# Kernel optimization log

Hardware: AMD Instinct MI355X
Metric: run time of the kernel (lower is better)

Reference implementation:

```python
import jax, jax.numpy as jnp
import numpy as np

H = 16          # heads_num
D = 1024        # model_dim
HD = D // H     # per-head dim
NEG = -1e9


def setup_inputs() -> dict:
    key = jax.random.key(0)
    ks = jax.random.split(key, 12)
    B, S = 4, 1024
    inp = {
        "q": jax.random.normal(ks[0], (B, S, D), jnp.float32),
        "k": jax.random.normal(ks[1], (B, S, D), jnp.float32),
        "v": jax.random.normal(ks[2], (B, S, D), jnp.float32),
        "mask": jnp.ones((B, 1, S), jnp.int32),
    }
    s = 1.0 / np.sqrt(D)
    inp["Wq"] = jax.random.normal(ks[3], (D, D), jnp.float32) * s
    inp["bq"] = jnp.zeros((D,), jnp.float32)
    inp["Wk"] = jax.random.normal(ks[4], (D, D), jnp.float32) * s
    inp["bk"] = jnp.zeros((D,), jnp.float32)
    inp["Wv"] = jax.random.normal(ks[5], (D, D), jnp.float32) * s
    inp["bv"] = jnp.zeros((D,), jnp.float32)
    inp["Wo"] = jax.random.normal(ks[6], (D, D), jnp.float32) * s
    inp["bo"] = jnp.zeros((D,), jnp.float32)
    return inp


def _split_heads(x, B):
    # [B, S, D] -> [B, H, S, HD]
    return x.reshape(B, -1, H, HD).transpose(0, 2, 1, 3)


def reference(q, k, v, mask, Wq, bq, Wk, bk, Wv, bv, Wo, bo):
    B = q.shape[0]
    qh = _split_heads(q @ Wq.T + bq, B)  # [B,H,Sq,HD]
    kh = _split_heads(k @ Wk.T + bk, B)  # [B,H,Sk,HD]
    vh = _split_heads(v @ Wv.T + bv, B)  # [B,H,Sk,HD]
    scores = jnp.einsum("bhqd,bhkd->bhqk", qh, kh) / np.sqrt(HD)
    # mask [B,1,Sk] -> unsqueeze head dim -> [B,1,1,Sk], broadcast over q and heads
    scores = jnp.where(mask[:, None] == 0, NEG, scores)
    attn = jax.nn.softmax(scores, axis=-1)  # dropout in eval mode = identity
    ctx = jnp.einsum("bhqk,bhkd->bhqd", attn, vh)
    out = ctx.transpose(0, 2, 1, 3).reshape(B, -1, D)
    return out @ Wo.T + bo
```

## Files before the change

kernel.cpp:

```cpp
#include <hip/hip_runtime.h>
#include <hip/hip_bf16.h>
#include <math.h>

typedef __bf16 bf16;
typedef __bf16 bf16x8 __attribute__((ext_vector_type(8)));
typedef __bf16 bf16x2 __attribute__((ext_vector_type(2)));
typedef float f32x4 __attribute__((ext_vector_type(4)));
typedef float f32x16 __attribute__((ext_vector_type(16)));

#define D_MODEL 1024
#define SEQ 1024
#define BATCH 4
#define NHEAD 16
#define MTOT (BATCH*SEQ)

#define QSCALE 0.18033688011112042f
#define MASKNEG -1e9f
#define EXP2(x) __builtin_amdgcn_exp2f(x)

__global__ void cast_all(const float* __restrict__ s0, const float* __restrict__ s1,
                         const float* __restrict__ s2, const float* __restrict__ s3,
                         const float* __restrict__ s4, const float* __restrict__ s5,
                         const float* __restrict__ s6,
                         bf16* d0, bf16* d1, bf16* d2, bf16* d3, bf16* d4, bf16* d5, bf16* d6) {
    int z = blockIdx.y;
    const float* s; bf16* d; int n;
    switch (z) {
        case 0: s = s0; d = d0; n = MTOT * D_MODEL; break;
        case 1: s = s1; d = d1; n = MTOT * D_MODEL; break;
        case 2: s = s2; d = d2; n = MTOT * D_MODEL; break;
        case 3: s = s3; d = d3; n = D_MODEL * D_MODEL; break;
        case 4: s = s4; d = d4; n = D_MODEL * D_MODEL; break;
        case 5: s = s5; d = d5; n = D_MODEL * D_MODEL; break;
        default: s = s6; d = d6; n = D_MODEL * D_MODEL; break;
    }
    int idx = (blockIdx.x * blockDim.x + threadIdx.x) * 8;
    int stride = gridDim.x * blockDim.x * 8;
    for (int i = idx; i < n; i += stride) {
        const float4* p = (const float4*)(s + i);
        float4 a = p[0], b = p[1];
        bf16x8 o;
        o[0] = (bf16)a.x; o[1] = (bf16)a.y; o[2] = (bf16)a.z; o[3] = (bf16)a.w;
        o[4] = (bf16)b.x; o[5] = (bf16)b.y; o[6] = (bf16)b.z; o[7] = (bf16)b.w;
        *(bf16x8*)(d + i) = o;
    }
}

template<typename OT, int MODE>
__global__ __launch_bounds__(256, 3)
void gemm_bt(const bf16* __restrict__ A0, const bf16* __restrict__ A1, const bf16* __restrict__ A2,
             const bf16* __restrict__ W0, const bf16* __restrict__ W1, const bf16* __restrict__ W2,
             const float* __restrict__ bias0, const float* __restrict__ bias1, const float* __restrict__ bias2,
             OT* __restrict__ O0, OT* __restrict__ O1, OT* __restrict__ O2) {
    constexpr int BK = 32;
    constexpr int K = D_MODEL;
    constexpr int NT = K / BK;
    __shared__ alignas(16) bf16 As[2][128 * BK];
    __shared__ alignas(16) bf16 Bs[2][128 * BK];

    int z = (MODE == 0) ? blockIdx.z : 0;
    const bf16* A = (z == 0) ? A0 : (z == 1) ? A1 : A2;
    const bf16* W = (z == 0) ? W0 : (z == 1) ? W1 : W2;
    const float* bias = (z == 0) ? bias0 : (z == 1) ? bias1 : bias2;
    OT* Out = (z == 0) ? O0 : (z == 1) ? O1 : O2;

    int tid = threadIdx.x;
    int lane = tid & 63, w = tid >> 6;
    int l15 = lane & 15, l4 = lane >> 4;
    int m0 = blockIdx.x * 128;
    int n0 = blockIdx.y * 128;
    int wm = w >> 1, wn = w & 1;

    f32x4 acc[4][4] = {};

    int srow = lane >> 2;
    int scol = (lane & 3) * 8;

    auto stage = [&](int buf, int kt) {
#pragma unroll
        for (int i = 0; i < 2; ++i) {
            int seg = w * 2 + i;
            int row = seg * 16 + srow;
            const bf16* srcA = A + (size_t)(m0 + row) * K + kt * BK + scol;
            const bf16* srcB = W + (size_t)(n0 + row) * K + kt * BK + scol;
            __builtin_amdgcn_global_load_lds(
                (const __attribute__((address_space(1))) void*)srcA,
                (__attribute__((address_space(3))) void*)(&As[buf][seg * 512]), 16, 0, 0);
            __builtin_amdgcn_global_load_lds(
                (const __attribute__((address_space(1))) void*)srcB,
                (__attribute__((address_space(3))) void*)(&Bs[buf][seg * 512]), 16, 0, 0);
        }
    };

    stage(0, 0);
    __syncthreads();

    for (int kt = 0; kt < NT; ++kt) {
        int cur = kt & 1;
        if (kt + 1 < NT) stage(cur ^ 1, kt + 1);

        const bf16* pa = &As[cur][(wm * 64 + l15) * BK + l4 * 8];
        const bf16* pb = &Bs[cur][(wn * 64 + l15) * BK + l4 * 8];
        bf16x8 af[4], bv[4];
#pragma unroll
        for (int m = 0; m < 4; ++m) af[m] = *(const bf16x8*)(pa + m * 16 * BK);
#pragma unroll
        for (int n = 0; n < 4; ++n) bv[n] = *(const bf16x8*)(pb + n * 16 * BK);
#pragma unroll
        for (int m = 0; m < 4; ++m)
#pragma unroll
            for (int n = 0; n < 4; ++n)
                acc[m][n] = __builtin_amdgcn_mfma_f32_16x16x32_bf16(af[m], bv[n], acc[m][n], 0, 0, 0);

        __syncthreads();
    }

    float bload[4];
#pragma unroll
    for (int n = 0; n < 4; ++n) bload[n] = bias[n0 + wn * 64 + n * 16 + l15];

    if (MODE == 0 && z == 2) {
#pragma unroll
        for (int m = 0; m < 4; ++m) {
            int row = m0 + wm * 64 + m * 16 + l4 * 4;
#pragma unroll
            for (int n = 0; n < 4; ++n) {
                int col = n0 + wn * 64 + n * 16 + l15;
                float bl = bload[n];
#pragma unroll
                for (int r = 0; r < 4; ++r) {
                    float vv = acc[m][n][r] + bl;
                    int rr = row + r;
                    int bb = rr >> 10, s = rr & 1023;
                    Out[((size_t)(bb * 1024 + col)) * 1024 + s] = (OT)vv;
                }
            }
        }
    } else {
        const float sc = (MODE == 0 && z == 0) ? QSCALE : 1.0f;
#pragma unroll
        for (int m = 0; m < 4; ++m) {
            int row = m0 + wm * 64 + m * 16 + l4 * 4;
#pragma unroll
            for (int n = 0; n < 4; ++n) {
                int col = n0 + wn * 64 + n * 16 + l15;
                float bl = bload[n];
#pragma unroll
                for (int r = 0; r < 4; ++r) {
                    float vv = (acc[m][n][r] + bl) * sc;
                    Out[(size_t)(row + r) * D_MODEL + col] = (OT)vv;
                }
            }
        }
    }
}

__device__ __forceinline__ unsigned pkbf(float lo, float hi2) {
    bf16x2 t; t[0] = (bf16)lo; t[1] = (bf16)hi2;
    return __builtin_bit_cast(unsigned, t);
}

__global__ __launch_bounds__(512, 4)
void attn_fwd(const bf16* __restrict__ Qp, const bf16* __restrict__ Kp,
              const bf16* __restrict__ VT, const int* __restrict__ maskp,
              bf16* __restrict__ ctx) {
    __shared__ alignas(16) unsigned char smem[69760];
    bf16* Kbuf = (bf16*)smem;
    bf16* Vbuf = (bf16*)(smem + 32768);
    float* madd2 = (float*)(smem + 65536);
    int* tflag = (int*)(smem + 69632);

    int tid = threadIdx.x;
    int lane = tid & 63, w = tid >> 6;
    int l31 = lane & 31, hi = lane >> 5;
    int hh = w >> 2, wl = w & 3;

    int fid = blockIdx.x;
    int xcd = fid & 7, idx = fid >> 3;
    int by = xcd * 8 + (idx >> 3);
    int bx = idx & 7;
    int b = by >> 4, h = by & 15;
    int q0 = bx * 128;

    {
        madd2[tid] = maskp[b * SEQ + tid] ? 0.f : MASKNEG;
        madd2[512 + tid] = maskp[b * SEQ + 512 + tid] ? 0.f : MASKNEG;
#pragma unroll
        for (int i = 0; i < 2; ++i) {
            int t = w * 2 + i;
            unsigned long long bl = __ballot(maskp[b * SEQ + t * 64 + lane] != 0);
            if (lane == 0) tflag[t] = (bl == ~0ull);
        }
    }

    bf16x8 qf[4];
    {
        const bf16* qb = Qp + ((size_t)(b * SEQ + q0 + wl * 32 + l31)) * D_MODEL + h * 64 + hi * 8;
#pragma unroll
        for (int ks = 0; ks < 4; ++ks) qf[ks] = *(const bf16x8*)(qb + ks * 16);
    }

    f32x16 oacc0 = {}, oacc1 = {};
    float lsum = 0.f;

    auto stage = [&](int buf, int t) {
        int kv0 = (hh * 8 + t) * 64;
        bf16* Kd = Kbuf + (size_t)(buf * 2 + hh) * 4096;
        bf16* Vd = Vbuf + (size_t)(buf * 2 + hh) * 4096;
#pragma unroll
        for (int i = 0; i < 2; ++i) {
            int seg = wl * 2 + i;
            int row = seg * 8 + (lane >> 3);
            int cs = ((lane & 7) ^ (row & 7)) * 8;
            const bf16* srcK = Kp + ((size_t)(b * SEQ + kv0 + row)) * D_MODEL + h * 64 + cs;
            __builtin_amdgcn_global_load_lds(
                (const __attribute__((address_space(1))) void*)srcK,
                (__attribute__((address_space(3))) void*)(Kd + seg * 512), 16, 0, 0);
            const bf16* srcV = VT + ((size_t)(b * 1024 + h * 64 + row)) * SEQ + kv0 + cs;
            __builtin_amdgcn_global_load_lds(
                (const __attribute__((address_space(1))) void*)srcV,
                (__attribute__((address_space(3))) void*)(Vd + seg * 512), 16, 0, 0);
        }
    };

    auto half_p = [&](f32x16& p, const float* mbh, int flag, const bf16* Vl, int ksb) -> float {
        float a0 = 0.f, a1 = 0.f, a2 = 0.f, a3 = 0.f;
        if (flag) {
#pragma unroll
            for (int g = 0; g < 4; ++g) {
                float s0 = 0.f;
#pragma unroll
                for (int c = 0; c < 4; ++c) {
                    int r = g * 4 + c;
                    float e = EXP2(p[r]);
                    p[r] = e; s0 += e;
                }
                if (g == 0) a0 = s0; else if (g == 1) a1 = s0;
                else if (g == 2) a2 = s0; else a3 = s0;
            }
        } else {
#pragma unroll
            for (int g = 0; g < 4; ++g) {
                f32x4 mk = *(const f32x4*)(mbh + g * 8 + hi * 4);
                float s0 = 0.f;
#pragma unroll
                for (int c = 0; c < 4; ++c) {
                    int r = g * 4 + c;
                    float e = EXP2(p[r] + mk[c]);
                    p[r] = e; s0 += e;
                }
                if (g == 0) a0 = s0; else if (g == 1) a1 = s0;
                else if (g == 2) a2 = s0; else a3 = s0;
            }
        }
        union FragU { bf16x8 v; unsigned u[4]; };
        FragU A0, A1;
#define PKSW(PV, RA, RB, DST)  { \
            unsigned a_ = pkbf(PV[RA], PV[(RA) + 1]); \
            unsigned b_ = pkbf(PV[RB], PV[(RB) + 1]); \
            auto rr_ = __builtin_amdgcn_permlane32_swap(a_, b_, false, false); \
            DST.u[((RA) & 3) >> 1] = rr_[0]; DST.u[(((RA) & 3) >> 1) + 2] = rr_[1]; }
        PKSW(p, 0, 4,  A0);
        PKSW(p, 2, 6,  A0);
        PKSW(p, 8, 12, A1);
        PKSW(p, 10, 14, A1);
#undef PKSW
        __builtin_amdgcn_s_setprio(1);
#pragma unroll
        for (int i = 0; i < 2; ++i) {
            int ks = ksb + i;
            bf16x8 pav = i ? A1.v : A0.v;
            int sl = ((2 * ks + hi) ^ (l31 & 7)) * 8;
            bf16x8 v0 = *(const bf16x8*)(&Vl[l31 * 64 + sl]);
            bf16x8 v1 = *(const bf16x8*)(&Vl[(32 + l31) * 64 + sl]);
            oacc0 = __builtin_amdgcn_mfma_f32_32x32x16_bf16(pav, v0, oacc0, 0, 0, 0);
            oacc1 = __builtin_amdgcn_mfma_f32_32x32x16_bf16(pav, v1, oacc1, 0, 0, 0);
        }
        __builtin_amdgcn_s_setprio(0);
        return (a0 + a1) + (a2 + a3);
    };

    stage(0, 0);
    __syncthreads();

    for (int t = 0; t < 8; ++t) {
        int cur = t & 1;
        if (t + 1 < 8) stage(cur ^ 1, t + 1);
        int kt = hh * 8 + t;
        const bf16* Kl = Kbuf + (size_t)(cur * 2 + hh) * 4096;
        const bf16* Vl = Vbuf + (size_t)(cur * 2 + hh) * 4096;
        const float* mb = &madd2[kt * 64];
        int flag = tflag[kt];

        float ts;
        {
            f32x16 p = {};
            __builtin_amdgcn_s_setprio(1);
#pragma unroll
            for (int ks = 0; ks < 4; ++ks) {
                int sl = ((2 * ks + hi) ^ (l31 & 7)) * 8;
                bf16x8 k0 = *(const bf16x8*)(&Kl[l31 * 64 + sl]);
                p = __builtin_amdgcn_mfma_f32_32x32x16_bf16(k0, qf[ks], p, 0, 0, 0);
            }
            __builtin_amdgcn_s_setprio(0);
            ts = half_p(p, mb, flag, Vl, 0);
        }
        {
            f32x16 p = {};
            __builtin_amdgcn_s_setprio(1);
#pragma unroll
            for (int ks = 0; ks < 4; ++ks) {
                int sl = ((2 * ks + hi) ^ (l31 & 7)) * 8;
                bf16x8 k1 = *(const bf16x8*)(&Kl[(32 + l31) * 64 + sl]);
                p = __builtin_amdgcn_mfma_f32_32x32x16_bf16(k1, qf[ks], p, 0, 0, 0);
            }
            __builtin_amdgcn_s_setprio(0);
            ts += half_p(p, mb + 32, flag, Vl, 2);
        }
        ts += __shfl_xor(ts, 32);
        lsum += ts;

        __syncthreads();
    }

    float* Omrg = (float*)smem;
    float* Lmrg = (float*)(smem + 32768);
    if (hh == 1) {
#pragma unroll
        for (int g = 0; g < 4; ++g) {
#pragma unroll
            for (int c = 0; c < 4; ++c) {
                int r = g * 4 + c;
                int q = c + g * 8 + hi * 4;
                Omrg[wl * 2048 + q * 64 + l31]      = oacc0[r];
                Omrg[wl * 2048 + q * 64 + 32 + l31] = oacc1[r];
            }
        }
        if (hi == 0) Lmrg[wl * 32 + l31] = lsum;
    }
    __syncthreads();
    if (hh == 0) {
        float ltot = lsum + Lmrg[wl * 32 + l31];
#pragma unroll
        for (int g = 0; g < 4; ++g) {
#pragma unroll
            for (int c = 0; c < 4; ++c) {
                int r = g * 4 + c;
                int q = c + g * 8 + hi * 4;
                float o0 = oacc0[r] + Omrg[wl * 2048 + q * 64 + l31];
                float o1 = oacc1[r] + Omrg[wl * 2048 + q * 64 + 32 + l31];
                float sden = __shfl(ltot, q);
                float inv = 1.0f / sden;
                int qg = q0 + wl * 32 + q;
                size_t base = ((size_t)(b * SEQ + qg)) * D_MODEL + h * 64;
                ctx[base + l31]      = (bf16)(o0 * inv);
                ctx[base + 32 + l31] = (bf16)(o1 * inv);
            }
        }
    }
}

extern "C" void kernel_launch(void* const* d_in, const int* in_sizes, int n_in,
                              void* d_out, int out_size, void* d_ws, size_t ws_size,
                              hipStream_t stream) {
    const float* q  = (const float*)d_in[0];
    const float* k  = (const float*)d_in[1];
    const float* v  = (const float*)d_in[2];
    const int* mask = (const int*)d_in[3];
    const float* Wq = (const float*)d_in[4];
    const float* bq = (const float*)d_in[5];
    const float* Wk = (const float*)d_in[6];
    const float* bk = (const float*)d_in[7];
    const float* Wv = (const float*)d_in[8];
    const float* bv = (const float*)d_in[9];
    const float* Wo = (const float*)d_in[10];
    const float* bo = (const float*)d_in[11];
    float* out = (float*)d_out;

    char* ws = (char*)d_ws;
    size_t szQKV = (size_t)MTOT * D_MODEL * sizeof(bf16);
    size_t szW = (size_t)D_MODEL * D_MODEL * sizeof(bf16);
    bf16* qb  = (bf16*)ws; ws += szQKV;
    bf16* kb  = (bf16*)ws; ws += szQKV;
    bf16* vb  = (bf16*)ws; ws += szQKV;
    bf16* Wqb = (bf16*)ws; ws += szW;
    bf16* Wkb = (bf16*)ws; ws += szW;
    bf16* Wvb = (bf16*)ws; ws += szW;
    bf16* Wob = (bf16*)ws; ws += szW;
    bf16* Qp  = (bf16*)ws; ws += szQKV;
    bf16* Kp  = (bf16*)ws; ws += szQKV;
    bf16* VT  = (bf16*)ws; ws += szQKV;
    bf16* ctx = (bf16*)ws; ws += szQKV;

    dim3 gc(512, 7, 1);
    cast_all<<<gc, 256, 0, stream>>>(q, k, v, Wq, Wk, Wv, Wo,
                                     qb, kb, vb, Wqb, Wkb, Wvb, Wob);

    dim3 g1(MTOT / 128, D_MODEL / 128, 3);
    gemm_bt<bf16, 0><<<g1, 256, 0, stream>>>(qb, kb, vb, Wqb, Wkb, Wvb,
                                             bq, bk, bv, Qp, Kp, VT);

    attn_fwd<<<dim3(512), 512, 0, stream>>>(Qp, Kp, VT, mask, ctx);

    dim3 g3(MTOT / 128, D_MODEL / 128, 1);
    gemm_bt<float, 1><<<g3, 256, 0, stream>>>(ctx, ctx, ctx, Wob, Wob, Wob,
                                              bo, bo, bo, out, out, out);
}
```

Baseline: 103.5 us.

## Fuse fp32-to-bf16 activation cast into QKV projection GEMM loads

The separate pass that cast the q/k/v activations to bf16 is removed. The QKV GEMM now streams fp32 activations straight into LDS with an XOR-swizzled layout and converts them to bf16 while building the MFMA fragments. This drops a full read-write round trip of three 16 MB activation tensors plus their bf16 staging buffers, and the cast kernel now only converts the weights. In exchange the QKV GEMM moves twice as many A bytes per tile, uses double the A LDS footprint, and does the conversion in its inner loop, so it may become more memory- or LDS-bound.

Measured after the change: 108.6 us. +5.0%, slower.

```diff
diff --git a/kernel.cpp b/kernel.cpp
--- a/kernel.cpp
+++ b/kernel.cpp
@@ -18,22 +18,18 @@
 #define MASKNEG -1e9f
 #define EXP2(x) __builtin_amdgcn_exp2f(x)
 
-__global__ void cast_all(const float* __restrict__ s0, const float* __restrict__ s1,
-                         const float* __restrict__ s2, const float* __restrict__ s3,
-                         const float* __restrict__ s4, const float* __restrict__ s5,
-                         const float* __restrict__ s6,
-                         bf16* d0, bf16* d1, bf16* d2, bf16* d3, bf16* d4, bf16* d5, bf16* d6) {
+__global__ void cast_w(const float* __restrict__ s0, const float* __restrict__ s1,
+                       const float* __restrict__ s2, const float* __restrict__ s3,
+                       bf16* d0, bf16* d1, bf16* d2, bf16* d3) {
     int z = blockIdx.y;
-    const float* s; bf16* d; int n;
+    const float* s; bf16* d;
     switch (z) {
-        case 0: s = s0; d = d0; n = MTOT * D_MODEL; break;
-        case 1: s = s1; d = d1; n = MTOT * D_MODEL; break;
-        case 2: s = s2; d = d2; n = MTOT * D_MODEL; break;
-        case 3: s = s3; d = d3; n = D_MODEL * D_MODEL; break;
-        case 4: s = s4; d = d4; n = D_MODEL * D_MODEL; break;
-        case 5: s = s5; d = d5; n = D_MODEL * D_MODEL; break;
-        default: s = s6; d = d6; n = D_MODEL * D_MODEL; break;
-    }
+        case 0: s = s0; d = d0; break;
+        case 1: s = s1; d = d1; break;
+        case 2: s = s2; d = d2; break;
+        default: s = s3; d = d3; break;
+    }
+    const int n = D_MODEL * D_MODEL;
     int idx = (blockIdx.x * blockDim.x + threadIdx.x) * 8;
     int stride = gridDim.x * blockDim.x * 8;
     for (int i = idx; i < n; i += stride) {
@@ -46,23 +42,22 @@
     }
 }
 
-template<typename OT, int MODE>
 __global__ __launch_bounds__(256, 3)
-void gemm_bt(const bf16* __restrict__ A0, const bf16* __restrict__ A1, const bf16* __restrict__ A2,
-             const bf16* __restrict__ W0, const bf16* __restrict__ W1, const bf16* __restrict__ W2,
-             const float* __restrict__ bias0, const float* __restrict__ bias1, const float* __restrict__ bias2,
-             OT* __restrict__ O0, OT* __restrict__ O1, OT* __restrict__ O2) {
+void gemm_qkv(const float* __restrict__ A0, const float* __restrict__ A1, const float* __restrict__ A2,
+              const bf16* __restrict__ W0, const bf16* __restrict__ W1, const bf16* __restrict__ W2,
+              const float* __restrict__ bias0, const float* __restrict__ bias1, const float* __restrict__ bias2,
+              bf16* __restrict__ O0, bf16* __restrict__ O1, bf16* __restrict__ O2) {
     constexpr int BK = 32;
     constexpr int K = D_MODEL;
     constexpr int NT = K / BK;
-    __shared__ alignas(16) bf16 As[2][128 * BK];
-    __shared__ alignas(16) bf16 Bs[2][128 * BK];
-
-    int z = (MODE == 0) ? blockIdx.z : 0;
-    const bf16* A = (z == 0) ? A0 : (z == 1) ? A1 : A2;
+    __shared__ alignas(16) float Asf[2][128 * BK];
+    __shared__ alignas(16) bf16  Bs[2][128 * BK];
+
+    int z = blockIdx.z;
+    const float* A = (z == 0) ? A0 : (z == 1) ? A1 : A2;
     const bf16* W = (z == 0) ? W0 : (z == 1) ? W1 : W2;
     const float* bias = (z == 0) ? bias0 : (z == 1) ? bias1 : bias2;
-    OT* Out = (z == 0) ? O0 : (z == 1) ? O1 : O2;
+    bf16* Out = (z == 0) ? O0 : (z == 1) ? O1 : O2;
 
     int tid = threadIdx.x;
     int lane = tid & 63, w = tid >> 6;
@@ -73,6 +68,122 @@
 
     f32x4 acc[4][4] = {};
 
+    int bsrow = lane >> 2;
+    int bscol = (lane & 3) * 8;
+    int arow8 = lane >> 3;
+    int acs = ((lane & 7) ^ (lane >> 3)) * 4;
+
+    auto stage = [&](int buf, int kt) {
+#pragma unroll
+        for (int i = 0; i < 4; ++i) {
+            int seg = w * 4 + i;
+            int row = seg * 8 + arow8;
+            const float* srcA = A + (size_t)(m0 + row) * K + kt * BK + acs;
+            __builtin_amdgcn_global_load_lds(
+                (const __attribute__((address_space(1))) void*)srcA,
+                (__attribute__((address_space(3))) void*)(&Asf[buf][seg * 256]), 16, 0, 0);
+        }
+#pragma unroll
+        for (int i = 0; i < 2; ++i) {
+            int seg = w * 2 + i;
+            int row = seg * 16 + bsrow;
+            const bf16* srcB = W + (size_t)(n0 + row) * K + kt * BK + bscol;
+            __builtin_amdgcn_global_load_lds(
+                (const __attribute__((address_space(1))) void*)srcB,
+                (__attribute__((address_space(3))) void*)(&Bs[buf][seg * 512]), 16, 0, 0);
+        }
+    };
+
+    stage(0, 0);
+    __syncthreads();
+
+    for (int kt = 0; kt < NT; ++kt) {
+        int cur = kt & 1;
+        if (kt + 1 < NT) stage(cur ^ 1, kt + 1);
+
+        bf16x8 af[4];
+#pragma unroll
+        for (int m = 0; m < 4; ++m) {
+            int r = wm * 64 + m * 16 + l15;
+            int p0 = (2 * l4) ^ (r & 7);
+            int p1 = (2 * l4 + 1) ^ (r & 7);
+            f32x4 a0 = *(const f32x4*)(&Asf[cur][r * BK + p0 * 4]);
+            f32x4 a1 = *(const f32x4*)(&Asf[cur][r * BK + p1 * 4]);
+            bf16x8 o;
+            o[0] = (bf16)a0[0]; o[1] = (bf16)a0[1]; o[2] = (bf16)a0[2]; o[3] = (bf16)a0[3];
+            o[4] = (bf16)a1[0]; o[5] = (bf16)a1[1]; o[6] = (bf16)a1[2]; o[7] = (bf16)a1[3];
+            af[m] = o;
+        }
+        const bf16* pb = &Bs[cur][(wn * 64 + l15) * BK + l4 * 8];
+        bf16x8 bv[4];
+#pragma unroll
+        for (int n = 0; n < 4; ++n) bv[n] = *(const bf16x8*)(pb + n * 16 * BK);
+#pragma unroll
+        for (int m = 0; m < 4; ++m)
+#pragma unroll
+            for (int n = 0; n < 4; ++n)
+                acc[m][n] = __builtin_amdgcn_mfma_f32_16x16x32_bf16(af[m], bv[n], acc[m][n], 0, 0, 0);
+
+        __syncthreads();
+    }
+
+    float bload[4];
+#pragma unroll
+    for (int n = 0; n < 4; ++n) bload[n] = bias[n0 + wn * 64 + n * 16 + l15];
+
+    if (z == 2) {
+#pragma unroll
+        for (int m = 0; m < 4; ++m) {
+            int row = m0 + wm * 64 + m * 16 + l4 * 4;
+#pragma unroll
+            for (int n = 0; n < 4; ++n) {
+                int col = n0 + wn * 64 + n * 16 + l15;
+                float bl = bload[n];
+#pragma unroll
+                for (int r = 0; r < 4; ++r) {
+                    float vv = acc[m][n][r] + bl;
+                    int rr = row + r;
+                    int bb = rr >> 10, s = rr & 1023;
+                    Out[((size_t)(bb * 1024 + col)) * 1024 + s] = (bf16)vv;
+                }
+            }
+        }
+    } else {
+        const float sc = (z == 0) ? QSCALE : 1.0f;
+#pragma unroll
+        for (int m = 0; m < 4; ++m) {
+            int row = m0 + wm * 64 + m * 16 + l4 * 4;
+#pragma unroll
+            for (int n = 0; n < 4; ++n) {
+                int col = n0 + wn * 64 + n * 16 + l15;
+                float bl = bload[n];
+#pragma unroll
+                for (int r = 0; r < 4; ++r) {
+                    float vv = (acc[m][n][r] + bl) * sc;
+                    Out[(size_t)(row + r) * D_MODEL + col] = (bf16)vv;
+                }
+            }
+        }
+    }
+}
+
+__global__ __launch_bounds__(256, 3)
+void gemm_out(const bf16* __restrict__ A, const bf16* __restrict__ W,
+              const float* __restrict__ bias, float* __restrict__ Out) {
+    constexpr int BK = 32;
+    constexpr int K = D_MODEL;
+    constexpr int NT = K / BK;
+    __shared__ alignas(16) bf16 As[2][128 * BK];
+    __shared__ alignas(16) bf16 Bs[2][128 * BK];
+
+    int tid = threadIdx.x;
+    int lane = tid & 63, w = tid >> 6;
+    int l15 = lane & 15, l4 = lane >> 4;
+    int m0 = blockIdx.x * 128;
+    int n0 = blockIdx.y * 128;
+    int wm = w >> 1, wn = w & 1;
+
+    f32x4 acc[4][4] = {};
     int srow = lane >> 2;
     int scol = (lane & 3) * 8;
 
@@ -118,39 +229,16 @@
     float bload[4];
 #pragma unroll
     for (int n = 0; n < 4; ++n) bload[n] = bias[n0 + wn * 64 + n * 16 + l15];
-
-    if (MODE == 0 && z == 2) {
-#pragma unroll
-        for (int m = 0; m < 4; ++m) {
-            int row = m0 + wm * 64 + m * 16 + l4 * 4;
-#pragma unroll
-            for (int n = 0; n < 4; ++n) {
-                int col = n0 + wn * 64 + n * 16 + l15;
-                float bl = bload[n];
-#pragma unroll
-                for (int r = 0; r < 4; ++r) {
-                    float vv = acc[m][n][r] + bl;
-                    int rr = row + r;
-                    int bb = rr >> 10, s = rr & 1023;
-                    Out[((size_t)(bb * 1024 + col)) * 1024 + s] = (OT)vv;
-                }
-            }
-        }
-    } else {
-        const float sc = (MODE == 0 && z == 0) ? QSCALE : 1.0f;
-#pragma unroll
-        for (int m = 0; m < 4; ++m) {
-            int row = m0 + wm * 64 + m * 16 + l4 * 4;
-#pragma unroll
-            for (int n = 0; n < 4; ++n) {
-                int col = n0 + wn * 64 + n * 16 + l15;
-                float bl = bload[n];
-#pragma unroll
-                for (int r = 0; r < 4; ++r) {
-                    float vv = (acc[m][n][r] + bl) * sc;
-                    Out[(size_t)(row + r) * D_MODEL + col] = (OT)vv;
-                }
-            }
+#pragma unroll
+    for (int m = 0; m < 4; ++m) {
+        int row = m0 + wm * 64 + m * 16 + l4 * 4;
+#pragma unroll
+        for (int n = 0; n < 4; ++n) {
+            int col = n0 + wn * 64 + n * 16 + l15;
+            float bl = bload[n];
+#pragma unroll
+            for (int r = 0; r < 4; ++r)
+                Out[(size_t)(row + r) * D_MODEL + col] = acc[m][n][r] + bl;
         }
     }
 }
@@ -380,9 +468,6 @@
     char* ws = (char*)d_ws;
     size_t szQKV = (size_t)MTOT * D_MODEL * sizeof(bf16);
     size_t szW = (size_t)D_MODEL * D_MODEL * sizeof(bf16);
-    bf16* qb  = (bf16*)ws; ws += szQKV;
-    bf16* kb  = (bf16*)ws; ws += szQKV;
-    bf16* vb  = (bf16*)ws; ws += szQKV;
     bf16* Wqb = (bf16*)ws; ws += szW;
     bf16* Wkb = (bf16*)ws; ws += szW;
     bf16* Wvb = (bf16*)ws; ws += szW;
@@ -392,17 +477,15 @@
     bf16* VT  = (bf16*)ws; ws += szQKV;
     bf16* ctx = (bf16*)ws; ws += szQKV;
 
-    dim3 gc(512, 7, 1);
-    cast_all<<<gc, 256, 0, stream>>>(q, k, v, Wq, Wk, Wv, Wo,
-                                     qb, kb, vb, Wqb, Wkb, Wvb, Wob);
+    dim3 gc(256, 4, 1);
+    cast_w<<<gc, 256, 0, stream>>>(Wq, Wk, Wv, Wo, Wqb, Wkb, Wvb, Wob);
 
     dim3 g1(MTOT / 128, D_MODEL / 128, 3);
-    gemm_bt<bf16, 0><<<g1, 256, 0, stream>>>(qb, kb, vb, Wqb, Wkb, Wvb,
-                                             bq, bk, bv, Qp, Kp, VT);
+    gemm_qkv<<<g1, 256, 0, stream>>>(q, k, v, Wqb, Wkb, Wvb,
+                                     bq, bk, bv, Qp, Kp, VT);
 
     attn_fwd<<<dim3(512), 512, 0, stream>>>(Qp, Kp, VT, mask, ctx);
 
     dim3 g3(MTOT / 128, D_MODEL / 128, 1);
-    gemm_bt<float, 1><<<g3, 256, 0, stream>>>(ctx, ctx, ctx, Wob, Wob, Wob,
-                                              bo, bo, bo, out, out, out);
-}
+    gemm_out<<<g3, 256, 0, stream>>>(ctx, Wob, bo, out);
+}
```

## Load GEMM operands directly from global into registers, dropping LDS staging

Applied to the files above, without the earlier changes.

Removes the LDS double buffer and the per-iteration barriers from the projection GEMM. Each wave now loads its A and W fragments straight from global memory into registers, with two register sets ping-ponged across k-steps, and raises wave priority around the MFMA block. Launch bounds drop to 2 blocks per CU so the extra registers fit. Loads shared between waves are no longer reused through LDS, which doubles global/L2 traffic and uses uncoalesced 16-byte row-strided accesses.

Result: slower. 165.8 us (+60.2%).

```diff
diff --git a/kernel.cpp b/kernel.cpp
--- a/kernel.cpp
+++ b/kernel.cpp
@@ -47,16 +47,13 @@
 }
 
 template<typename OT, int MODE>
-__global__ __launch_bounds__(256, 3)
+__global__ __launch_bounds__(256, 2)
 void gemm_bt(const bf16* __restrict__ A0, const bf16* __restrict__ A1, const bf16* __restrict__ A2,
              const bf16* __restrict__ W0, const bf16* __restrict__ W1, const bf16* __restrict__ W2,
              const float* __restrict__ bias0, const float* __restrict__ bias1, const float* __restrict__ bias2,
              OT* __restrict__ O0, OT* __restrict__ O1, OT* __restrict__ O2) {
-    constexpr int BK = 32;
     constexpr int K = D_MODEL;
-    constexpr int NT = K / BK;
-    __shared__ alignas(16) bf16 As[2][128 * BK];
-    __shared__ alignas(16) bf16 Bs[2][128 * BK];
+    constexpr int NT = K / 32;
 
     int z = (MODE == 0) ? blockIdx.z : 0;
     const bf16* A = (z == 0) ? A0 : (z == 1) ? A1 : A2;
@@ -71,48 +68,37 @@
     int n0 = blockIdx.y * 128;
     int wm = w >> 1, wn = w & 1;
 
+    const bf16* Ab = A + (size_t)(m0 + wm * 64 + l15) * K + l4 * 8;
+    const bf16* Bb = W + (size_t)(n0 + wn * 64 + l15) * K + l4 * 8;
+
     f32x4 acc[4][4] = {};
-
-    int srow = lane >> 2;
-    int scol = (lane & 3) * 8;
-
-    auto stage = [&](int buf, int kt) {
-#pragma unroll
-        for (int i = 0; i < 2; ++i) {
-            int seg = w * 2 + i;
-            int row = seg * 16 + srow;
-            const bf16* srcA = A + (size_t)(m0 + row) * K + kt * BK + scol;
-            const bf16* srcB = W + (size_t)(n0 + row) * K + kt * BK + scol;
-            __builtin_amdgcn_global_load_lds(
-                (const __attribute__((address_space(1))) void*)srcA,
-                (__attribute__((address_space(3))) void*)(&As[buf][seg * 512]), 16, 0, 0);
-            __builtin_amdgcn_global_load_lds(
-                (const __attribute__((address_space(1))) void*)srcB,
-                (__attribute__((address_space(3))) void*)(&Bs[buf][seg * 512]), 16, 0, 0);
-        }
+    bf16x8 a0[4], b0[4], a1[4], b1[4];
+
+    auto load = [&](bf16x8* av, bf16x8* bv, int kt) {
+#pragma unroll
+        for (int m = 0; m < 4; ++m)
+            av[m] = *(const bf16x8*)(Ab + (size_t)m * 16 * K + kt * 32);
+#pragma unroll
+        for (int n = 0; n < 4; ++n)
+            bv[n] = *(const bf16x8*)(Bb + (size_t)n * 16 * K + kt * 32);
     };
-
-    stage(0, 0);
-    __syncthreads();
-
-    for (int kt = 0; kt < NT; ++kt) {
-        int cur = kt & 1;
-        if (kt + 1 < NT) stage(cur ^ 1, kt + 1);
-
-        const bf16* pa = &As[cur][(wm * 64 + l15) * BK + l4 * 8];
-        const bf16* pb = &Bs[cur][(wn * 64 + l15) * BK + l4 * 8];
-        bf16x8 af[4], bv[4];
-#pragma unroll
-        for (int m = 0; m < 4; ++m) af[m] = *(const bf16x8*)(pa + m * 16 * BK);
-#pragma unroll
-        for (int n = 0; n < 4; ++n) bv[n] = *(const bf16x8*)(pb + n * 16 * BK);
+    auto compute = [&](const bf16x8* av, const bf16x8* bv) {
+        __builtin_amdgcn_s_setprio(1);
 #pragma unroll
         for (int m = 0; m < 4; ++m)
 #pragma unroll
             for (int n = 0; n < 4; ++n)
-                acc[m][n] = __builtin_amdgcn_mfma_f32_16x16x32_bf16(af[m], bv[n], acc[m][n], 0, 0, 0);
-
-        __syncthreads();
+                acc[m][n] = __builtin_amdgcn_mfma_f32_16x16x32_bf16(av[m], bv[n], acc[m][n], 0, 0, 0);
+        __builtin_amdgcn_s_setprio(0);
+    };
+
+    load(a0, b0, 0);
+#pragma unroll 1
+    for (int kt2 = 0; kt2 < NT / 2; ++kt2) {
+        load(a1, b1, 2 * kt2 + 1);
+        compute(a0, b0);
+        if (kt2 + 1 < NT / 2) load(a0, b0, 2 * kt2 + 2);
+        compute(a1, b1);
     }
 
     float bload[4];
```

## Add 256x256 8-wave QKV GEMM with quadrant-interleaved LDS pipelining

Applied to the files above, without the earlier changes.

Replaces the fused QKV projection GEMM with a new kernel using 256x256 tiles, 512 threads, BK=64, XOR-swizzled LDS, and a hand-scheduled pipeline. The pipeline interleaves half-tile global-to-LDS loads with MFMA quadrants, using explicit vmcnt/lgkmcnt waits and setprio. The aim is more data reuse per tile and better overlap of memory with matrix math. In exchange, the grid gets smaller (192 blocks) and register pressure rises, and the hand-tuned wait counts are fragile. The output GEMM is split into its own simpler kernel.

New measurement: 106.2 us. 2.6% more time.

```diff
diff --git a/kernel.cpp b/kernel.cpp
--- a/kernel.cpp
+++ b/kernel.cpp
@@ -17,6 +17,10 @@
 #define QSCALE 0.18033688011112042f
 #define MASKNEG -1e9f
 #define EXP2(x) __builtin_amdgcn_exp2f(x)
+
+#define GLL(SRC, DST) __builtin_amdgcn_global_load_lds( \
+    (const __attribute__((address_space(1))) void*)(SRC), \
+    (__attribute__((address_space(3))) void*)(DST), 16, 0, 0)
 
 __global__ void cast_all(const float* __restrict__ s0, const float* __restrict__ s1,
                          const float* __restrict__ s2, const float* __restrict__ s3,
@@ -46,23 +50,183 @@
     }
 }
 
-template<typename OT, int MODE>
+#define VMBAR  do { asm volatile("s_waitcnt vmcnt(6)" ::: "memory"); \
+                    __builtin_amdgcn_s_barrier(); \
+                    __builtin_amdgcn_sched_barrier(0); } while (0)
+#define LGKM0  do { asm volatile("s_waitcnt lgkmcnt(0)" ::: "memory"); \
+                    __builtin_amdgcn_sched_barrier(0); } while (0)
+
+__global__ __launch_bounds__(512, 2)
+void gemm_qkv8(const bf16* __restrict__ A0p, const bf16* __restrict__ A1p, const bf16* __restrict__ A2p,
+               const bf16* __restrict__ W0, const bf16* __restrict__ W1, const bf16* __restrict__ W2,
+               const float* __restrict__ bias0, const float* __restrict__ bias1, const float* __restrict__ bias2,
+               bf16* __restrict__ O0, bf16* __restrict__ O1, bf16* __restrict__ O2) {
+    constexpr int K = D_MODEL;
+    __shared__ bf16 Al[2][2][8192];
+    __shared__ bf16 Bl[2][2][8192];
+
+    int z = blockIdx.z;
+    const bf16* A = (z == 0) ? A0p : (z == 1) ? A1p : A2p;
+    const bf16* W = (z == 0) ? W0 : (z == 1) ? W1 : W2;
+    const float* bias = (z == 0) ? bias0 : (z == 1) ? bias1 : bias2;
+    bf16* Out = (z == 0) ? O0 : (z == 1) ? O1 : O2;
+
+    int tid = threadIdx.x;
+    int l = tid & 63, w = tid >> 6;
+    int l15 = l & 15, l4 = l >> 4;
+    int wm = w >> 2, wn = w & 3;
+    int m0 = blockIdx.x * 256;
+    int n0 = blockIdx.y * 256;
+
+    f32x4 acc[8][4] = {};
+
+    int srf = l >> 3;
+    int scc = (l & 7) ^ (srf & 7);
+
+    auto stageA = [&](int buf, int H, int kt) {
+#pragma unroll
+        for (int j = 0; j < 2; ++j) {
+            int r = (w * 2 + j) * 8 + srf;
+            const bf16* src = A + (size_t)(m0 + H * 128 + r) * K + kt * 64 + scc * 8;
+            GLL(src, &Al[buf][H][(w * 2 + j) * 512]);
+        }
+    };
+    auto stageB = [&](int buf, int H, int kt) {
+#pragma unroll
+        for (int j = 0; j < 2; ++j) {
+            int r = (w * 2 + j) * 8 + srf;
+            const bf16* src = W + (size_t)(n0 + H * 128 + r) * K + kt * 64 + scc * 8;
+            GLL(src, &Bl[buf][H][(w * 2 + j) * 512]);
+        }
+    };
+
+    bf16x8 a[4][2], bf0[2][2], bf1[2][2];
+
+    auto loadA = [&](int buf, int H) {
+#pragma unroll
+        for (int j2 = 0; j2 < 4; ++j2) {
+            int rh = (2 * j2 + wm) * 16 + l15;
+#pragma unroll
+            for (int ks = 0; ks < 2; ++ks) {
+                int cp = (ks * 4 + l4) ^ (l15 & 7);
+                a[j2][ks] = *(const bf16x8*)&Al[buf][H][rh * 64 + cp * 8];
+            }
+        }
+    };
+    auto loadB = [&](bf16x8 bdst[2][2], int buf, int H) {
+#pragma unroll
+        for (int n2 = 0; n2 < 2; ++n2) {
+            int rh = (4 * n2 + wn) * 16 + l15;
+#pragma unroll
+            for (int ks = 0; ks < 2; ++ks) {
+                int cp = (ks * 4 + l4) ^ (l15 & 7);
+                bdst[n2][ks] = *(const bf16x8*)&Bl[buf][H][rh * 64 + cp * 8];
+            }
+        }
+    };
+
+#define MMAQ(M, N, BSET) do { \
+        __builtin_amdgcn_s_setprio(1); \
+        _Pragma("unroll") \
+        for (int j2 = 0; j2 < 4; ++j2) \
+        _Pragma("unroll") \
+        for (int n2 = 0; n2 < 2; ++n2) \
+        _Pragma("unroll") \
+        for (int ks = 0; ks < 2; ++ks) \
+            acc[(M)*4 + j2][(N)*2 + n2] = __builtin_amdgcn_mfma_f32_16x16x32_bf16( \
+                a[j2][ks], BSET[n2][ks], acc[(M)*4 + j2][(N)*2 + n2], 0, 0, 0); \
+        __builtin_amdgcn_s_setprio(0); \
+    } while (0)
+
+    stageA(0, 0, 0); stageB(0, 0, 0);
+    stageA(0, 1, 0); stageB(0, 1, 0);
+    stageA(1, 0, 1); stageB(1, 0, 1);
+
+#pragma unroll 1
+    for (int i = 0; i < 8; ++i) {
+        int t1 = 2 * i + 1, s0 = 2 * i + 2, s1 = 2 * i + 3;
+        bool pre = (i < 7);
+        VMBAR;
+        loadA(0, 0); loadB(bf0, 0, 0);
+        stageA(1, 1, t1);
+        LGKM0; MMAQ(0, 0, bf0);
+        VMBAR;
+        loadB(bf1, 0, 1);
+        stageB(1, 1, t1);
+        LGKM0; MMAQ(0, 1, bf1);
+        VMBAR;
+        loadA(0, 1);
+        if (pre) stageA(0, 0, s0);
+        LGKM0; MMAQ(1, 0, bf0);
+        VMBAR;
+        if (pre) stageB(0, 0, s0);
+        MMAQ(1, 1, bf1);
+        VMBAR;
+        loadA(1, 0); loadB(bf0, 1, 0);
+        if (pre) stageA(0, 1, s0);
+        LGKM0; MMAQ(0, 0, bf0);
+        VMBAR;
+        loadB(bf1, 1, 1);
+        if (pre) stageB(0, 1, s0);
+        LGKM0; MMAQ(0, 1, bf1);
+        VMBAR;
+        loadA(1, 1);
+        if (pre) stageA(1, 0, s1);
+        LGKM0; MMAQ(1, 0, bf0);
+        VMBAR;
+        if (pre) stageB(1, 0, s1);
+        MMAQ(1, 1, bf1);
+    }
+#undef MMAQ
+
+    float bload[4];
+#pragma unroll
+    for (int n = 0; n < 4; ++n) bload[n] = bias[n0 + (4 * n + wn) * 16 + l15];
+
+    if (z == 2) {
+#pragma unroll
+        for (int j = 0; j < 8; ++j) {
+            int row = m0 + (2 * j + wm) * 16 + l4 * 4;
+#pragma unroll
+            for (int n = 0; n < 4; ++n) {
+                int col = n0 + (4 * n + wn) * 16 + l15;
+                float bl = bload[n];
+#pragma unroll
+                for (int r = 0; r < 4; ++r) {
+                    float vv = acc[j][n][r] + bl;
+                    int rr = row + r;
+                    int bb = rr >> 10, s = rr & 1023;
+                    Out[((size_t)(bb * 1024 + col)) * 1024 + s] = (bf16)vv;
+                }
+            }
+        }
+    } else {
+        const float sc = (z == 0) ? QSCALE : 1.0f;
+#pragma unroll
+        for (int j = 0; j < 8; ++j) {
+            int row = m0 + (2 * j + wm) * 16 + l4 * 4;
+#pragma unroll
+            for (int n = 0; n < 4; ++n) {
+                int col = n0 + (4 * n + wn) * 16 + l15;
+                float bl = bload[n];
+#pragma unroll
+                for (int r = 0; r < 4; ++r) {
+                    float vv = (acc[j][n][r] + bl) * sc;
+                    Out[(size_t)(row + r) * D_MODEL + col] = (bf16)vv;
+                }
+            }
+        }
+    }
+}
+
 __global__ __launch_bounds__(256, 3)
-void gemm_bt(const bf16* __restrict__ A0, const bf16* __restrict__ A1, const bf16* __restrict__ A2,
-             const bf16* __restrict__ W0, const bf16* __restrict__ W1, const bf16* __restrict__ W2,
-             const float* __restrict__ bias0, const float* __restrict__ bias1, const float* __restrict__ bias2,
-             OT* __restrict__ O0, OT* __restrict__ O1, OT* __restrict__ O2) {
+void gemm_out(const bf16* __restrict__ A, const bf16* __restrict__ W,
+              const float* __restrict__ bias, float* __restrict__ Out) {
     constexpr int BK = 32;
     constexpr int K = D_MODEL;
     constexpr int NT = K / BK;
     __shared__ alignas(16) bf16 As[2][128 * BK];
     __shared__ alignas(16) bf16 Bs[2][128 * BK];
-
-    int z = (MODE == 0) ? blockIdx.z : 0;
-    const bf16* A = (z == 0) ? A0 : (z == 1) ? A1 : A2;
-    const bf16* W = (z == 0) ? W0 : (z == 1) ? W1 : W2;
-    const float* bias = (z == 0) ? bias0 : (z == 1) ? bias1 : bias2;
-    OT* Out = (z == 0) ? O0 : (z == 1) ? O1 : O2;
 
     int tid = threadIdx.x;
     int lane = tid & 63, w = tid >> 6;
@@ -72,7 +236,6 @@
     int wm = w >> 1, wn = w & 1;
 
     f32x4 acc[4][4] = {};
-
     int srow = lane >> 2;
     int scol = (lane & 3) * 8;
 
@@ -83,12 +246,8 @@
             int row = seg * 16 + srow;
             const bf16* srcA = A + (size_t)(m0 + row) * K + kt * BK + scol;
             const bf16* srcB = W + (size_t)(n0 + row) * K + kt * BK + scol;
-            __builtin_amdgcn_global_load_lds(
-                (const __attribute__((address_space(1))) void*)srcA,
-                (__attribute__((address_space(3))) void*)(&As[buf][seg * 512]), 16, 0, 0);
-            __builtin_amdgcn_global_load_lds(
-                (const __attribute__((address_space(1))) void*)srcB,
-                (__attribute__((address_space(3))) void*)(&Bs[buf][seg * 512]), 16, 0, 0);
+            GLL(srcA, &As[buf][seg * 512]);
+            GLL(srcB, &Bs[buf][seg * 512]);
         }
     };
 
@@ -118,39 +277,16 @@
     float bload[4];
 #pragma unroll
     for (int n = 0; n < 4; ++n) bload[n] = bias[n0 + wn * 64 + n * 16 + l15];
-
-    if (MODE == 0 && z == 2) {
-#pragma unroll
-        for (int m = 0; m < 4; ++m) {
-            int row = m0 + wm * 64 + m * 16 + l4 * 4;
-#pragma unroll
-            for (int n = 0; n < 4; ++n) {
-                int col = n0 + wn * 64 + n * 16 + l15;
-                float bl = bload[n];
-#pragma unroll
-                for (int r = 0; r < 4; ++r) {
-                    float vv = acc[m][n][r] + bl;
-                    int rr = row + r;
-                    int bb = rr >> 10, s = rr & 1023;
-                    Out[((size_t)(bb * 1024 + col)) * 1024 + s] = (OT)vv;
-                }
-            }
-        }
-    } else {
-        const float sc = (MODE == 0 && z == 0) ? QSCALE : 1.0f;
-#pragma unroll
-        for (int m = 0; m < 4; ++m) {
-            int row = m0 + wm * 64 + m * 16 + l4 * 4;
-#pragma unroll
-            for (int n = 0; n < 4; ++n) {
-                int col = n0 + wn * 64 + n * 16 + l15;
-                float bl = bload[n];
-#pragma unroll
-                for (int r = 0; r < 4; ++r) {
-                    float vv = (acc[m][n][r] + bl) * sc;
-                    Out[(size_t)(row + r) * D_MODEL + col] = (OT)vv;
-                }
-            }
+#pragma unroll
+    for (int m = 0; m < 4; ++m) {
+        int row = m0 + wm * 64 + m * 16 + l4 * 4;
+#pragma unroll
+        for (int n = 0; n < 4; ++n) {
+            int col = n0 + wn * 64 + n * 16 + l15;
+            float bl = bload[n];
+#pragma unroll
+            for (int r = 0; r < 4; ++r)
+                Out[(size_t)(row + r) * D_MODEL + col] = acc[m][n][r] + bl;
         }
     }
 }
@@ -213,13 +349,9 @@
             int row = seg * 8 + (lane >> 3);
             int cs = ((lane & 7) ^ (row & 7)) * 8;
             const bf16* srcK = Kp + ((size_t)(b * SEQ + kv0 + row)) * D_MODEL + h * 64 + cs;
-            __builtin_amdgcn_global_load_lds(
-                (const __attribute__((address_space(1))) void*)srcK,
-                (__attribute__((address_space(3))) void*)(Kd + seg * 512), 16, 0, 0);
+            GLL(srcK, Kd + seg * 512);
             const bf16* srcV = VT + ((size_t)(b * 1024 + h * 64 + row)) * SEQ + kv0 + cs;
-            __builtin_amdgcn_global_load_lds(
-                (const __attribute__((address_space(1))) void*)srcV,
-                (__attribute__((address_space(3))) void*)(Vd + seg * 512), 16, 0, 0);
+            GLL(srcV, Vd + seg * 512);
         }
     };
 
@@ -396,13 +528,12 @@
     cast_all<<<gc, 256, 0, stream>>>(q, k, v, Wq, Wk, Wv, Wo,
                                      qb, kb, vb, Wqb, Wkb, Wvb, Wob);
 
-    dim3 g1(MTOT / 128, D_MODEL / 128, 3);
-    gemm_bt<bf16, 0><<<g1, 256, 0, stream>>>(qb, kb, vb, Wqb, Wkb, Wvb,
-                                             bq, bk, bv, Qp, Kp, VT);
+    dim3 g1(MTOT / 256, D_MODEL / 256, 3);
+    gemm_qkv8<<<g1, 512, 0, stream>>>(qb, kb, vb, Wqb, Wkb, Wvb,
+                                      bq, bk, bv, Qp, Kp, VT);
 
     attn_fwd<<<dim3(512), 512, 0, stream>>>(Qp, Kp, VT, mask, ctx);
 
     dim3 g3(MTOT / 128, D_MODEL / 128, 1);
-    gemm_bt<float, 1><<<g3, 256, 0, stream>>>(ctx, ctx, ctx, Wob, Wob, Wob,
-                                              bo, bo, bo, out, out, out);
+    gemm_out<<<g3, 256, 0, stream>>>(ctx, Wob, bo, out);
 }
```
